# Kernel optimization log

Measured on AMD Instinct MI355X. Metric: run time of the kernel, lower is better.

Reference implementation:

```python
import jax, jax.numpy as jnp
import numpy as np

B, T, F, H = 64, 128, 188, 16  # batch, time, in_features, feature_embed_dim
N_CONT = F - 11  # features 11.. are continuous (177)


def setup_inputs() -> dict:
    key = jax.random.key(0)
    ks = jax.random.split(key, 14)
    s = 1.0 / np.sqrt(H)  # nn.Linear default init scale
    u = lambda k, shape: jax.random.uniform(k, shape, jnp.float32, -s, s)
    return {
        "x": jax.random.normal(ks[0], (B, T, F * H), jnp.float32),
        # grouped per-feature Linear weights, grouped by output dim
        "W2a": u(ks[1], (4, H, 2)),  "b2a": u(ks[2], (4, 2)),   # features 0-3
        "W3":  u(ks[3], (2, H, 3)),  "b3":  u(ks[4], (2, 3)),   # features 4-5
        "W4":  u(ks[5], (1, H, 4)),  "b4":  u(ks[6], (1, 4)),   # feature 6
        "W6":  u(ks[7], (1, H, 6)),  "b6":  u(ks[8], (1, 6)),   # feature 7
        "W7":  u(ks[9], (3, H, 7)),  "b7":  u(ks[10], (3, 7)),  # features 8-10
        "Wc":  u(ks[11], (N_CONT, H, 2)), "bc": u(ks[12], (N_CONT, 2)),  # features 11..
        "eps": jax.random.normal(ks[13], (B * T, N_CONT), jnp.float32),  # normal-sampling noise
    }


def _cat_argmax(xg, W, b):
    # softmax then argmax == argmax of logits
    logits = jnp.einsum('nfd,fdo->nfo', xg, W) + b
    return jnp.argmax(logits, axis=-1).astype(jnp.float32)


def reference(x, W2a, b2a, W3, b3, W4, b4, W6, b6, W7, b7, Wc, bc, eps):
    xr = x.reshape(B * T, F, H)
    cats = jnp.concatenate([
        _cat_argmax(xr[:, 0:4],  W2a, b2a),
        _cat_argmax(xr[:, 4:6],  W3,  b3),
        _cat_argmax(xr[:, 6:7],  W4,  b4),
        _cat_argmax(xr[:, 7:8],  W6,  b6),
        _cat_argmax(xr[:, 8:11], W7,  b7),
    ], axis=1)  # [N, 11]
    dec = jnp.einsum('nfd,fdo->nfo', xr[:, 11:], Wc) + bc  # [N, 177, 2]
    mean = jnp.tanh(dec[..., 0])
    std = jax.nn.sigmoid(dec[..., 1])
    samp = mean + std * eps  # reparameterized t.normal(mean, std)
    outs = jnp.concatenate([cats, samp], axis=1)  # [N, 188]
    return outs.reshape(B, T, F)
```

## Files before the change

kernel.cpp:

```cpp
#include <hip/hip_runtime.h>
#include <hip/hip_bf16.h>
#include <cmath>

#define NROWS   8192
#define FDIM    188
#define HDIM    16
#define NCONT   177
#define NCAT    11
#define XSTRIDE 3008
#define CHUNK   8
#define NB      (NROWS / CHUNK)


__global__ __launch_bounds__(256)
void tab_dec_kernel(const float* __restrict__ x,
                    const float* __restrict__ W2a, const float* __restrict__ b2a,
                    const float* __restrict__ W3,  const float* __restrict__ b3,
                    const float* __restrict__ W4,  const float* __restrict__ b4,
                    const float* __restrict__ W6,  const float* __restrict__ b6,
                    const float* __restrict__ W7,  const float* __restrict__ b7,
                    const float* __restrict__ Wc,  const float* __restrict__ bc,
                    const float* __restrict__ eps,
                    float* __restrict__ out)
{
    const int t  = blockIdx.x * blockDim.x + threadIdx.x;
    const int TC = NCONT * NB;

    if (t < TC) {
        const int nb = t / NCONT;
        const int cf = t - nb * NCONT;

        float w[32];
        const float4* wp = reinterpret_cast<const float4*>(Wc + cf * 32);
        #pragma unroll
        for (int k = 0; k < 8; ++k) {
            float4 v = wp[k];
            w[4*k+0] = v.x; w[4*k+1] = v.y; w[4*k+2] = v.z; w[4*k+3] = v.w;
        }
        const float b0 = bc[cf * 2 + 0];
        const float b1 = bc[cf * 2 + 1];

        const int n0 = nb * CHUNK;
        const float* xbase = x + (size_t)n0 * XSTRIDE + (size_t)(NCAT + cf) * HDIM;

        #pragma unroll 2
        for (int j = 0; j < CHUNK; ++j) {
            const float4* xq = reinterpret_cast<const float4*>(xbase + (size_t)j * XSTRIDE);
            float4 a0 = xq[0], a1 = xq[1], a2 = xq[2], a3 = xq[3];
            float xv[16] = { a0.x, a0.y, a0.z, a0.w,
                             a1.x, a1.y, a1.z, a1.w,
                             a2.x, a2.y, a2.z, a2.w,
                             a3.x, a3.y, a3.z, a3.w };
            float m = b0, s = b1;
            #pragma unroll
            for (int d = 0; d < 16; ++d) {
                m = fmaf(xv[d], w[2*d],     m);
                s = fmaf(xv[d], w[2*d + 1], s);
            }
            float mc   = fminf(fmaxf(m, -10.0f), 10.0f);
            float mean = 1.0f - 2.0f / (__expf(2.0f * mc) + 1.0f);
            float stdv = 1.0f / (1.0f + __expf(-s));
            const int n = n0 + j;
            out[(size_t)n * FDIM + NCAT + cf] =
                fmaf(stdv, eps[(size_t)n * NCONT + cf], mean);
        }
    } else if (t < TC + NCAT * NB) {
        const int tt = t - TC;
        const int nb = tt / NCAT;
        const int f  = tt - nb * NCAT;

        const float *W, *bb;
        int odim;
        if (f < 4)      { W = W2a + f * HDIM * 2;      bb = b2a + f * 2; odim = 2; }
        else if (f < 6) { W = W3 + (f - 4) * HDIM * 3; bb = b3 + (f - 4) * 3; odim = 3; }
        else if (f < 7) { W = W4;                      bb = b4;          odim = 4; }
        else if (f < 8) { W = W6;                      bb = b6;          odim = 6; }
        else            { W = W7 + (f - 8) * HDIM * 7; bb = b7 + (f - 8) * 7; odim = 7; }

        const int n0 = nb * CHUNK;
        for (int j = 0; j < CHUNK; ++j) {
            const int n = n0 + j;
            const float4* xq = reinterpret_cast<const float4*>(
                x + (size_t)n * XSTRIDE + (size_t)f * HDIM);
            float4 a0 = xq[0], a1 = xq[1], a2 = xq[2], a3 = xq[3];
            float xv[16] = { a0.x, a0.y, a0.z, a0.w,
                             a1.x, a1.y, a1.z, a1.w,
                             a2.x, a2.y, a2.z, a2.w,
                             a3.x, a3.y, a3.z, a3.w };
            float best = -1e30f;
            int   bi   = 0;
            for (int o = 0; o < odim; ++o) {
                float acc = bb[o];
                #pragma unroll
                for (int d = 0; d < 16; ++d) acc = fmaf(xv[d], W[d * odim + o], acc);
                if (acc > best) { best = acc; bi = o; }
            }
            out[(size_t)n * FDIM + f] = (float)bi;
        }
    }
}

extern "C" void kernel_launch(void* const* d_in, const int* in_sizes, int n_in,
                              void* d_out, int out_size, void* d_ws, size_t ws_size,
                              hipStream_t stream) {
    const float* x   = (const float*)d_in[0];
    const float* W2a = (const float*)d_in[1];
    const float* b2a = (const float*)d_in[2];
    const float* W3  = (const float*)d_in[3];
    const float* b3  = (const float*)d_in[4];
    const float* W4  = (const float*)d_in[5];
    const float* b4  = (const float*)d_in[6];
    const float* W6  = (const float*)d_in[7];
    const float* b6  = (const float*)d_in[8];
    const float* W7  = (const float*)d_in[9];
    const float* b7  = (const float*)d_in[10];
    const float* Wc  = (const float*)d_in[11];
    const float* bc  = (const float*)d_in[12];
    const float* eps = (const float*)d_in[13];
    float* out = (float*)d_out;

    const int total_threads = (NCONT + NCAT) * NB;
    dim3 grid((total_threads + 255) / 256), block(256);
    hipLaunchKernelGGL(tab_dec_kernel, grid, block, 0, stream,
                       x, W2a, b2a, W3, b3, W4, b4, W6, b6, W7, b7, Wc, bc, eps, out);
}
```

Measured before the change: 208.3 us.

## Split into per-element continuous and categorical kernels, drop row chunking

The single kernel, in which each thread looped over 8 rows, is replaced by two kernels. Each continuous kernel thread handles one (row, feature) pair; the categorical kernel likewise handles one (row, categorical feature). This multiplies the number of threads and outstanding memory requests, to improve latency hiding on a memory-bound streaming read of x. The cost is that each thread reloads its weight vector (cached) and there is one extra kernel launch.

```diff
diff --git a/kernel.cpp b/kernel.cpp
--- a/kernel.cpp
+++ b/kernel.cpp
@@ -8,96 +8,92 @@
 #define NCONT   177
 #define NCAT    11
 #define XSTRIDE 3008
-#define CHUNK   8
-#define NB      (NROWS / CHUNK)
-
 
 __global__ __launch_bounds__(256)
-void tab_dec_kernel(const float* __restrict__ x,
+void tab_cont_kernel(const float* __restrict__ x,
+                     const float* __restrict__ Wc, const float* __restrict__ bc,
+                     const float* __restrict__ eps,
+                     float* __restrict__ out)
+{
+    const int t = blockIdx.x * blockDim.x + threadIdx.x;
+    const int n  = t / NCONT;
+    const int cf = t - n * NCONT;
+
+    const float4* wp = reinterpret_cast<const float4*>(Wc + cf * 32);
+    float4 w0 = wp[0], w1 = wp[1], w2 = wp[2], w3 = wp[3];
+    float4 w4 = wp[4], w5 = wp[5], w6 = wp[6], w7 = wp[7];
+
+    const float2 bb = reinterpret_cast<const float2*>(bc)[cf];
+    const float  ev = eps[(size_t)n * NCONT + cf];
+
+    const float4* xq = reinterpret_cast<const float4*>(
+        x + (size_t)n * XSTRIDE + (size_t)(NCAT + cf) * HDIM);
+    float4 a0 = xq[0], a1 = xq[1], a2 = xq[2], a3 = xq[3];
+
+    float m = bb.x, s = bb.y;
+    m = fmaf(a0.x, w0.x, m); s = fmaf(a0.x, w0.y, s);
+    m = fmaf(a0.y, w0.z, m); s = fmaf(a0.y, w0.w, s);
+    m = fmaf(a0.z, w1.x, m); s = fmaf(a0.z, w1.y, s);
+    m = fmaf(a0.w, w1.z, m); s = fmaf(a0.w, w1.w, s);
+    m = fmaf(a1.x, w2.x, m); s = fmaf(a1.x, w2.y, s);
+    m = fmaf(a1.y, w2.z, m); s = fmaf(a1.y, w2.w, s);
+    m = fmaf(a1.z, w3.x, m); s = fmaf(a1.z, w3.y, s);
+    m = fmaf(a1.w, w3.z, m); s = fmaf(a1.w, w3.w, s);
+    m = fmaf(a2.x, w4.x, m); s = fmaf(a2.x, w4.y, s);
+    m = fmaf(a2.y, w4.z, m); s = fmaf(a2.y, w4.w, s);
+    m = fmaf(a2.z, w5.x, m); s = fmaf(a2.z, w5.y, s);
+    m = fmaf(a2.w, w5.z, m); s = fmaf(a2.w, w5.w, s);
+    m = fmaf(a3.x, w6.x, m); s = fmaf(a3.x, w6.y, s);
+    m = fmaf(a3.y, w6.z, m); s = fmaf(a3.y, w6.w, s);
+    m = fmaf(a3.z, w7.x, m); s = fmaf(a3.z, w7.y, s);
+    m = fmaf(a3.w, w7.z, m); s = fmaf(a3.w, w7.w, s);
+
+    float mc   = fminf(fmaxf(m, -10.0f), 10.0f);
+    float mean = 1.0f - 2.0f / (__expf(2.0f * mc) + 1.0f);
+    float stdv = 1.0f / (1.0f + __expf(-s));
+
+    out[(size_t)n * FDIM + NCAT + cf] = fmaf(stdv, ev, mean);
+}
+
+__global__ __launch_bounds__(256)
+void tab_cat_kernel(const float* __restrict__ x,
                     const float* __restrict__ W2a, const float* __restrict__ b2a,
                     const float* __restrict__ W3,  const float* __restrict__ b3,
                     const float* __restrict__ W4,  const float* __restrict__ b4,
                     const float* __restrict__ W6,  const float* __restrict__ b6,
                     const float* __restrict__ W7,  const float* __restrict__ b7,
-                    const float* __restrict__ Wc,  const float* __restrict__ bc,
-                    const float* __restrict__ eps,
                     float* __restrict__ out)
 {
-    const int t  = blockIdx.x * blockDim.x + threadIdx.x;
-    const int TC = NCONT * NB;
+    const int t = blockIdx.x * blockDim.x + threadIdx.x;
+    if (t >= NROWS * NCAT) return;
+    const int n = t / NCAT;
+    const int f = t - n * NCAT;
 
-    if (t < TC) {
-        const int nb = t / NCONT;
-        const int cf = t - nb * NCONT;
+    const float4* xq = reinterpret_cast<const float4*>(
+        x + (size_t)n * XSTRIDE + (size_t)f * HDIM);
+    float4 a0 = xq[0], a1 = xq[1], a2 = xq[2], a3 = xq[3];
+    float xv[16] = { a0.x, a0.y, a0.z, a0.w,
+                     a1.x, a1.y, a1.z, a1.w,
+                     a2.x, a2.y, a2.z, a2.w,
+                     a3.x, a3.y, a3.z, a3.w };
 
-        float w[32];
-        const float4* wp = reinterpret_cast<const float4*>(Wc + cf * 32);
+    const float *W, *bb;
+    int odim;
+    if (f < 4)      { W = W2a + f * HDIM * 2;      bb = b2a + f * 2;      odim = 2; }
+    else if (f < 6) { W = W3 + (f - 4) * HDIM * 3; bb = b3 + (f - 4) * 3; odim = 3; }
+    else if (f < 7) { W = W4;                      bb = b4;               odim = 4; }
+    else if (f < 8) { W = W6;                      bb = b6;               odim = 6; }
+    else            { W = W7 + (f - 8) * HDIM * 7; bb = b7 + (f - 8) * 7; odim = 7; }
+
+    float best = -1e30f;
+    int   bi   = 0;
+    for (int o = 0; o < odim; ++o) {
+        float acc = bb[o];
         #pragma unroll
-        for (int k = 0; k < 8; ++k) {
-            float4 v = wp[k];
-            w[4*k+0] = v.x; w[4*k+1] = v.y; w[4*k+2] = v.z; w[4*k+3] = v.w;
-        }
-        const float b0 = bc[cf * 2 + 0];
-        const float b1 = bc[cf * 2 + 1];
-
-        const int n0 = nb * CHUNK;
-        const float* xbase = x + (size_t)n0 * XSTRIDE + (size_t)(NCAT + cf) * HDIM;
-
-        #pragma unroll 2
-        for (int j = 0; j < CHUNK; ++j) {
-            const float4* xq = reinterpret_cast<const float4*>(xbase + (size_t)j * XSTRIDE);
-            float4 a0 = xq[0], a1 = xq[1], a2 = xq[2], a3 = xq[3];
-            float xv[16] = { a0.x, a0.y, a0.z, a0.w,
-                             a1.x, a1.y, a1.z, a1.w,
-                             a2.x, a2.y, a2.z, a2.w,
-                             a3.x, a3.y, a3.z, a3.w };
-            float m = b0, s = b1;
-            #pragma unroll
-            for (int d = 0; d < 16; ++d) {
-                m = fmaf(xv[d], w[2*d],     m);
-                s = fmaf(xv[d], w[2*d + 1], s);
-            }
-            float mc   = fminf(fmaxf(m, -10.0f), 10.0f);
-            float mean = 1.0f - 2.0f / (__expf(2.0f * mc) + 1.0f);
-            float stdv = 1.0f / (1.0f + __expf(-s));
-            const int n = n0 + j;
-            out[(size_t)n * FDIM + NCAT + cf] =
-                fmaf(stdv, eps[(size_t)n * NCONT + cf], mean);
-        }
-    } else if (t < TC + NCAT * NB) {
-        const int tt = t - TC;
-        const int nb = tt / NCAT;
-        const int f  = tt - nb * NCAT;
-
-        const float *W, *bb;
-        int odim;
-        if (f < 4)      { W = W2a + f * HDIM * 2;      bb = b2a + f * 2; odim = 2; }
-        else if (f < 6) { W = W3 + (f - 4) * HDIM * 3; bb = b3 + (f - 4) * 3; odim = 3; }
-        else if (f < 7) { W = W4;                      bb = b4;          odim = 4; }
-        else if (f < 8) { W = W6;                      bb = b6;          odim = 6; }
-        else            { W = W7 + (f - 8) * HDIM * 7; bb = b7 + (f - 8) * 7; odim = 7; }
-
-        const int n0 = nb * CHUNK;
-        for (int j = 0; j < CHUNK; ++j) {
-            const int n = n0 + j;
-            const float4* xq = reinterpret_cast<const float4*>(
-                x + (size_t)n * XSTRIDE + (size_t)f * HDIM);
-            float4 a0 = xq[0], a1 = xq[1], a2 = xq[2], a3 = xq[3];
-            float xv[16] = { a0.x, a0.y, a0.z, a0.w,
-                             a1.x, a1.y, a1.z, a1.w,
-                             a2.x, a2.y, a2.z, a2.w,
-                             a3.x, a3.y, a3.z, a3.w };
-            float best = -1e30f;
-            int   bi   = 0;
-            for (int o = 0; o < odim; ++o) {
-                float acc = bb[o];
-                #pragma unroll
-                for (int d = 0; d < 16; ++d) acc = fmaf(xv[d], W[d * odim + o], acc);
-                if (acc > best) { best = acc; bi = o; }
-            }
-            out[(size_t)n * FDIM + f] = (float)bi;
-        }
+        for (int d = 0; d < 16; ++d) acc = fmaf(xv[d], W[d * odim + o], acc);
+        if (acc > best) { best = acc; bi = o; }
     }
+    out[(size_t)n * FDIM + f] = (float)bi;
 }
 
 extern "C" void kernel_launch(void* const* d_in, const int* in_sizes, int n_in,
@@ -119,8 +115,8 @@
     const float* eps = (const float*)d_in[13];
     float* out = (float*)d_out;
 
-    const int total_threads = (NCONT + NCAT) * NB;
-    dim3 grid((total_threads + 255) / 256), block(256);
-    hipLaunchKernelGGL(tab_dec_kernel, grid, block, 0, stream,
-                       x, W2a, b2a, W3, b3, W4, b4, W6, b6, W7, b7, Wc, bc, eps, out);
+    hipLaunchKernelGGL(tab_cont_kernel, dim3(NROWS * NCONT / 256), dim3(256), 0, stream,
+                       x, Wc, bc, eps, out);
+    hipLaunchKernelGGL(tab_cat_kernel, dim3(NROWS * NCAT / 256), dim3(256), 0, stream,
+                       x, W2a, b2a, W3, b3, W4, b4, W6, b6, W7, b7, out);
 }
```

Measured after the change: 190.4 us. -8.6%, faster.
